# Performance work log

Measured on AMD Instinct MI355X. Metric: run time of the kernel, lower is better.

Reference implementation:

```python
import jax, jax.numpy as jnp
import numpy as np

B, L, C, H = 1, 2048, 2048, 16
D = C // H
EPS = 1e-6
W0 = 30.0  # SIREN frequency

def rmsnorm(x, w, eps=EPS):
    return x * jax.lax.rsqrt(jnp.mean(x * x, axis=-1, keepdims=True) + eps) * w

def depth_rope(x, depth, base=10000.0):
    # same rotation for all positions, angle set by scalar layer depth
    d = x.shape[-1]
    half = d // 2
    freqs = 1.0 / base ** (jnp.arange(half, dtype=x.dtype) / half)
    ang = depth * freqs
    cos, sin = jnp.cos(ang), jnp.sin(ang)
    x1, x2 = x[..., :half], x[..., half:2 * half]
    return jnp.concatenate([x1 * cos - x2 * sin, x1 * sin + x2 * cos], axis=-1)

def setup_inputs() -> dict:
    key = jax.random.key(0)
    ks = jax.random.split(key, 13)
    s = 1.0 / np.sqrt(C)
    inp = {
        'x':  jax.random.normal(ks[0], (B, L, C), jnp.float32),
        'h0': jax.random.normal(ks[1], (B, L, C), jnp.float32),
        'h1': jax.random.normal(ks[2], (B, L, C), jnp.float32),
        'h2': jax.random.normal(ks[3], (B, L, C), jnp.float32),
        'Wq': jax.random.normal(ks[4], (C, C), jnp.float32) * s,
        'Wk': jax.random.normal(ks[5], (C, C), jnp.float32) * s,
        'Wv': jax.random.normal(ks[6], (C, C), jnp.float32) * s,
        'Wo': jax.random.normal(ks[7], (C, C), jnp.float32) * s,
        'qn_w': jnp.ones((D,), jnp.float32),
        'kn_w': jnp.ones((D,), jnp.float32),
        'on_w': jnp.ones((C,), jnp.float32),
        'sw1': jax.random.normal(ks[8], (1, C), jnp.float32),
        'sb1': jax.random.normal(ks[9], (C,), jnp.float32) * 0.01,
        'sw2': jax.random.normal(ks[10], (C, C), jnp.float32) * s,
        'sb2': jnp.zeros((C,), jnp.float32),
    }
    return inp

def reference(x, h0, h1, h2, Wq, Wk, Wv, Wo, qn_w, kn_w, on_w, sw1, sb1, sw2, sb2):
    history = [h0, h1, h2]
    q_src = history[-1]                      # [B,L,C]
    q_depth = len(history) - 1
    # Q path: proj -> per-head RMSNorm -> depth RoPE
    q = jnp.einsum('blc,oc->blo', q_src, Wq).reshape(B, L, H, D)
    q = depth_rope(rmsnorm(q, qn_w), q_depth)
    # K/V path over prior history entries (each with its own depth)
    k_parts, v_parts = [], []
    for depth_idx, kv in enumerate(history[:-1]):
        k_i = jnp.einsum('blc,oc->blo', kv, Wk).reshape(B, L, H, D)
        v_i = jnp.einsum('blc,oc->blo', kv, Wv).reshape(B, L, H, D)
        k_parts.append(depth_rope(rmsnorm(k_i, kn_w), depth_idx))
        v_parts.append(v_i)
    k = jnp.concatenate(k_parts, axis=1)     # [B,Lkv,H,D]
    v = jnp.concatenate(v_parts, axis=1)
    # full SDPA, default scale D^-0.5
    scores = jnp.einsum('bqhd,bkhd->bhqk', q, k) * (D ** -0.5)
    attn = jax.nn.softmax(scores, axis=-1)
    out = jnp.einsum('bhqk,bkhd->bqhd', attn, v).reshape(B, L, C)
    out = jnp.einsum('blc,oc->blo', out, Wo)
    # SIREN upsample to (L,): target length == L -> identity interpolation
    # plus sine-activated coordinate MLP (implicit positional field)
    coords = jnp.linspace(-1.0, 1.0, L, dtype=x.dtype)[:, None]   # [L,1]
    pos = jnp.sin(W0 * (coords @ sw1 + sb1)) @ sw2 + sb2           # [L,C]
    out = out + pos[None]
    return x + rmsnorm(out, on_w)
```

## Files before the change

kernel.cpp:

```cpp
#include <hip/hip_runtime.h>
#include <hip/hip_fp16.h>

#define LQ 2048
#define CDIM 2048
#define NHEAD 16
#define HDIM 128
#define LKEY 4096

typedef _Float16 f16x8 __attribute__((ext_vector_type(8)));
typedef float f32x4 __attribute__((ext_vector_type(4)));

#define GLOAD_LDS16(g, s) __builtin_amdgcn_global_load_lds( \
    (const __attribute__((address_space(1))) void*)(g),     \
    (__attribute__((address_space(3))) void*)(s), 16, 0, 0)

#define MFMA16(a, b, c) __builtin_amdgcn_mfma_f32_16x16x32_f16(a, b, c, 0, 0, 0)

__device__ __forceinline__ void storeC(float* p, float v) { *p = v; }
__device__ __forceinline__ void storeC(__half* p, float v) { *p = __float2half(v); }
__device__ __forceinline__ float toF(float v) { return v; }
__device__ __forceinline__ float toF(__half v) { return __half2float(v); }

template <typename OutT>
__global__ __launch_bounds__(256, 2) void gemm_bt(
    const __half* __restrict__ A, const __half* __restrict__ B,
    OutT* __restrict__ C, int lda, int ldb, int ldc, int K)
{
    __shared__ __align__(16) __half lA[128 * 64];
    __shared__ __align__(16) __half lB[128 * 64];
    const int tid  = threadIdx.x;
    const int lane = tid & 63;
    const int wave = tid >> 6;
    const int bm = blockIdx.x, bn = blockIdx.y;
    const int r = tid >> 3;
    const int g = tid & 7;
    const __half* gA = A + (long)(bm * 128 + r) * lda + ((g ^ (r & 7)) << 3);
    const __half* gB = B + (long)(bn * 128 + r) * ldb + ((g ^ (r & 7)) << 3);
    __half* lAp = lA + tid * 8;
    __half* lBp = lB + tid * 8;
    const int wr = (wave & 1) << 6;
    const int wc = (wave >> 1) << 6;
    const int l15 = lane & 15, quad = lane >> 4;

    f32x4 acc[4][4] = {};

    for (int kt = 0; kt < K; kt += 64) {
#pragma unroll
        for (int i = 0; i < 4; ++i) {
            GLOAD_LDS16(gA + (long)i * 32 * lda, lAp + i * 2048);
            GLOAD_LDS16(gB + (long)i * 32 * ldb, lBp + i * 2048);
        }
        gA += 64; gB += 64;
        __syncthreads();
#pragma unroll
        for (int kk = 0; kk < 2; ++kk) {
            f16x8 af[4], bfr[4];
#pragma unroll
            for (int mi = 0; mi < 4; ++mi) {
                const int m = wr + mi * 16 + l15;
                const int kg = kk * 4 + quad;
                af[mi] = *(const f16x8*)&lA[m * 64 + ((kg ^ (m & 7)) << 3)];
            }
#pragma unroll
            for (int ni = 0; ni < 4; ++ni) {
                const int n = wc + ni * 16 + l15;
                const int kg = kk * 4 + quad;
                bfr[ni] = *(const f16x8*)&lB[n * 64 + ((kg ^ (n & 7)) << 3)];
            }
#pragma unroll
            for (int mi = 0; mi < 4; ++mi)
#pragma unroll
                for (int ni = 0; ni < 4; ++ni)
                    acc[mi][ni] = MFMA16(af[mi], bfr[ni], acc[mi][ni]);
        }
        __syncthreads();
    }
    const int row0 = bm * 128 + wr + quad * 4;
    const int col0 = bn * 128 + wc + l15;
#pragma unroll
    for (int mi = 0; mi < 4; ++mi)
#pragma unroll
        for (int ni = 0; ni < 4; ++ni)
#pragma unroll
            for (int rx = 0; rx < 4; ++rx)
                storeC(&C[(long)(row0 + mi * 16 + rx) * ldc + col0 + ni * 16],
                       acc[mi][ni][rx]);
}

__global__ __launch_bounds__(256, 2) void attn_tile(
    const __half* __restrict__ Qf,
    const __half* __restrict__ Kf,
    const __half* __restrict__ Vt,
    float* __restrict__ Opart,
    float* __restrict__ lsum)
{
    __shared__ __align__(16) __half lK[64 * 128];
    __shared__ __align__(16) __half lV[128 * 64];
    __shared__ __align__(16) __half pL[4 * 2 * 16 * 72];

    const int tid  = threadIdx.x;
    const int lane = tid & 63;
    const int wave = tid >> 6;
    const int l15  = lane & 15;
    const int quad = lane >> 4;
    const int h  = blockIdx.y >> 1;
    const int kc = blockIdx.y & 1;
    const int q0 = blockIdx.x * 128 + wave * 32;

    f16x8 aq[2][4];
#pragma unroll
    for (int mt = 0; mt < 2; ++mt)
#pragma unroll
        for (int ks = 0; ks < 4; ++ks)
            aq[mt][ks] = *(const f16x8*)&Qf[(long)(q0 + mt * 16 + l15) * CDIM +
                                            h * HDIM + ks * 32 + quad * 8];

    const int rK = tid >> 4;
    const int gK = tid & 15;
    const __half* srcK = Kf + (long)(kc * 2048 + rK) * 4096 + h * HDIM +
                         ((gK ^ (rK & 15)) << 3);
    const int rV = tid >> 3;
    const int gV = tid & 7;
    const __half* srcV = Vt + (long)(h * HDIM + rV) * (long)LKEY + kc * 2048 +
                         ((gV ^ (rV & 7)) << 3);
    __half* dstK = lK + tid * 8;
    __half* dstV = lV + tid * 8;

    f32x4 accO[2][8] = {};
    f32x4 l_acc[2] = {};

    for (int st = 0; st < 32; ++st) {
#pragma unroll
        for (int i = 0; i < 4; ++i) {
            GLOAD_LDS16(srcK + (long)(st * 64 + i * 16) * 4096, dstK + i * 2048);
            GLOAD_LDS16(srcV + (long)i * 32 * LKEY + st * 64, dstV + i * 2048);
        }
        __syncthreads();
        f32x4 s[2][4];
#pragma unroll
        for (int mt = 0; mt < 2; ++mt)
#pragma unroll
            for (int nt = 0; nt < 4; ++nt)
                s[mt][nt] = (f32x4){-10.f, -10.f, -10.f, -10.f};
#pragma unroll
        for (int nt = 0; nt < 4; ++nt) {
            const int n = nt * 16 + l15;
#pragma unroll
            for (int ks = 0; ks < 4; ++ks) {
                const f16x8 kf = *(const f16x8*)
                    &lK[n * 128 + (((ks * 4 + quad) ^ (n & 15)) << 3)];
                s[0][nt] = MFMA16(aq[0][ks], kf, s[0][nt]);
                s[1][nt] = MFMA16(aq[1][ks], kf, s[1][nt]);
            }
        }
#pragma unroll
        for (int mt = 0; mt < 2; ++mt)
#pragma unroll
            for (int nt = 0; nt < 4; ++nt)
#pragma unroll
                for (int r2 = 0; r2 < 4; ++r2) {
                    const float p = __builtin_amdgcn_exp2f(s[mt][nt][r2]);
                    l_acc[mt][r2] += p;
                    pL[((wave * 2 + mt) * 16 + quad * 4 + r2) * 72 +
                       nt * 16 + l15] = __float2half(p);
                }
        f16x8 ap[2][2];
#pragma unroll
        for (int mt = 0; mt < 2; ++mt) {
            ap[mt][0] = *(const f16x8*)&pL[((wave * 2 + mt) * 16 + l15) * 72 + quad * 8];
            ap[mt][1] = *(const f16x8*)&pL[((wave * 2 + mt) * 16 + l15) * 72 + 32 + quad * 8];
        }
#pragma unroll
        for (int nt2 = 0; nt2 < 8; ++nt2) {
            const int n2 = nt2 * 16 + l15;
            const f16x8 v0 = *(const f16x8*)&lV[n2 * 64 + ((quad ^ (n2 & 7)) << 3)];
            const f16x8 v1 = *(const f16x8*)&lV[n2 * 64 + (((4 + quad) ^ (n2 & 7)) << 3)];
            accO[0][nt2] = MFMA16(ap[0][0], v0, accO[0][nt2]);
            accO[0][nt2] = MFMA16(ap[0][1], v1, accO[0][nt2]);
            accO[1][nt2] = MFMA16(ap[1][0], v0, accO[1][nt2]);
            accO[1][nt2] = MFMA16(ap[1][1], v1, accO[1][nt2]);
        }
        __syncthreads();
    }

#pragma unroll
    for (int mt = 0; mt < 2; ++mt)
#pragma unroll
        for (int r2 = 0; r2 < 4; ++r2) {
            float v = l_acc[mt][r2];
            v += __shfl_xor(v, 1);
            v += __shfl_xor(v, 2);
            v += __shfl_xor(v, 4);
            v += __shfl_xor(v, 8);
            if (l15 == 0)
                atomicAdd(&lsum[h * LQ + q0 + mt * 16 + quad * 4 + r2], v);
        }
    float* Cp = Opart + (long)kc * LQ * CDIM + h * HDIM;
#pragma unroll
    for (int mt = 0; mt < 2; ++mt)
#pragma unroll
        for (int nt2 = 0; nt2 < 8; ++nt2)
#pragma unroll
            for (int rx = 0; rx < 4; ++rx)
                Cp[(long)(q0 + mt * 16 + quad * 4 + rx) * CDIM + nt2 * 16 + l15] =
                    accO[mt][nt2][rx];
}

__global__ __launch_bounds__(256) void merge_o(
    const float* __restrict__ Op, const float* __restrict__ lsum,
    __half* __restrict__ a2)
{
    const int row = blockIdx.x;
    const int c0  = threadIdx.x * 8;
    const float inv = 1.0f / lsum[(c0 >> 7) * LQ + row];
    const float* p0 = Op + (long)row * CDIM + c0;
    const float* p1 = p0 + (long)LQ * CDIM;
    union { f16x8 v; _Float16 e[8]; } o;
#pragma unroll
    for (int j = 0; j < 8; ++j)
        o.e[j] = (_Float16)((p0[j] + p1[j]) * inv);
    *(f16x8*)&a2[(long)row * 4096 + c0] = o.v;
}

__global__ __launch_bounds__(256) void norm_rope(
    __half* __restrict__ X, const float* __restrict__ w,
    int stride, int nrows, int kmode, float oscale)
{
    const int gid  = blockIdx.x * 4 + (threadIdx.x >> 6);
    const int lane = threadIdx.x & 63;
    const int row  = gid >> 4;
    const int h    = gid & 15;
    if (row >= nrows) return;
    __half* p = X + (long)row * stride + h * HDIM;
    float x1 = __half2float(p[lane]);
    float x2 = __half2float(p[lane + 64]);
    float ss = x1 * x1 + x2 * x2;
#pragma unroll
    for (int off = 1; off < 64; off <<= 1) ss += __shfl_xor(ss, off);
    const float rn = rsqrtf(ss * (1.0f / 128.0f) + 1e-6f);
    x1 *= rn * w[lane];
    x2 *= rn * w[lane + 64];
    const int depth = kmode ? (row < LQ ? 0 : 1) : 2;
    const float freq = exp2f(-(float)lane * 0.20762050593045702f);
    const float ang = (float)depth * freq;
    float sn, cs;
    __sincosf(ang, &sn, &cs);
    p[lane]      = __float2half((x1 * cs - x2 * sn) * oscale);
    p[lane + 64] = __float2half((x1 * sn + x2 * cs) * oscale);
}

__global__ void cast_h4(const float* __restrict__ in, __half* __restrict__ out, int n) {
    const int i = (blockIdx.x * 256 + threadIdx.x) << 2;
    if (i >= n) return;
    const float4 v = *(const float4*)&in[i];
    out[i]     = __float2half(v.x);
    out[i + 1] = __float2half(v.y);
    out[i + 2] = __float2half(v.z);
    out[i + 3] = __float2half(v.w);
}

__global__ void cast_wo(const float* __restrict__ in, __half* __restrict__ out) {
    const int idx = blockIdx.x * 256 + threadIdx.x;
    const int o = idx >> 11, c = idx & 2047;
    out[((long)o << 12) + c] = __float2half(in[idx]);
}

template <typename InT>
__global__ __launch_bounds__(256) void transpose_h(
    const InT* __restrict__ in, long inStride, long inOff,
    __half* __restrict__ out, long outStride, long outOff)
{
    __shared__ float t[64][65];
    const long r0 = (long)blockIdx.x * 64;
    const long c0 = (long)blockIdx.y * 64;
    const int tj = threadIdx.x & 63;
    const int ti = threadIdx.x >> 6;
#pragma unroll
    for (int it = 0; it < 16; ++it) {
        const int i = it * 4 + ti;
        t[i][tj] = toF(in[(r0 + i) * inStride + inOff + c0 + tj]);
    }
    __syncthreads();
#pragma unroll
    for (int it = 0; it < 16; ++it) {
        const int i = it * 4 + ti;
        out[(c0 + i) * outStride + outOff + r0 + tj] = __float2half(t[tj][i]);
    }
}

__global__ void sin_feat(const float* __restrict__ sw1, const float* __restrict__ sb1,
                         __half* __restrict__ a2) {
    const int idx = blockIdx.x * 256 + threadIdx.x;
    const int l = idx >> 11, c = idx & 2047;
    const float coord = -1.0f + (2.0f / 2047.0f) * (float)l;
    const float v = sinf(30.0f * (coord * sw1[c] + sb1[c]));
    a2[((long)l << 12) + 2048 + c] = __float2half(v);
}

__global__ __launch_bounds__(256) void final_norm(
    const float* __restrict__ out2, const float* __restrict__ x,
    const float* __restrict__ sb2, const float* __restrict__ on_w,
    float* __restrict__ y)
{
    const int row = blockIdx.x;
    const float* o = out2 + (long)row * CDIM;
    float v[8];
    float ss = 0.f;
#pragma unroll
    for (int i = 0; i < 8; ++i) {
        const int c = threadIdx.x + i * 256;
        const float t = o[c] + sb2[c];
        v[i] = t;
        ss += t * t;
    }
#pragma unroll
    for (int off = 1; off < 64; off <<= 1) ss += __shfl_xor(ss, off);
    __shared__ float red[4];
    const int lane = threadIdx.x & 63, wv = threadIdx.x >> 6;
    if (lane == 0) red[wv] = ss;
    __syncthreads();
    const float tot = red[0] + red[1] + red[2] + red[3];
    const float rn = rsqrtf(tot * (1.0f / 2048.0f) + 1e-6f);
#pragma unroll
    for (int i = 0; i < 8; ++i) {
        const int c = threadIdx.x + i * 256;
        y[(long)row * CDIM + c] = x[(long)row * CDIM + c] + v[i] * rn * on_w[c];
    }
}

extern "C" void kernel_launch(void* const* d_in, const int* in_sizes, int n_in,
                              void* d_out, int out_size, void* d_ws, size_t ws_size,
                              hipStream_t stream) {
    const float* x    = (const float*)d_in[0];
    const float* h0   = (const float*)d_in[1];
    const float* h1   = (const float*)d_in[2];
    const float* h2   = (const float*)d_in[3];
    const float* Wq   = (const float*)d_in[4];
    const float* Wk   = (const float*)d_in[5];
    const float* Wv   = (const float*)d_in[6];
    const float* Wo   = (const float*)d_in[7];
    const float* qn_w = (const float*)d_in[8];
    const float* kn_w = (const float*)d_in[9];
    const float* on_w = (const float*)d_in[10];
    const float* sw1  = (const float*)d_in[11];
    const float* sb1  = (const float*)d_in[12];
    const float* sw2  = (const float*)d_in[13];
    const float* sb2  = (const float*)d_in[14];
    float* y = (float*)d_out;

    const size_t MB = 1ull << 20;
    char* w = (char*)d_ws;
    __half* xq  = (__half*)(w);
    __half* xkv = (__half*)(w + 8 * MB);
    __half* wqh = (__half*)(w + 24 * MB);
    __half* wkv = (__half*)(w + 32 * MB);
    __half* qf  = (__half*)(w + 48 * MB);
    __half* kvf = (__half*)(w + 56 * MB);
    __half* vT  = (__half*)(w + 88 * MB);
    __half* a2  = (__half*)(w + 104 * MB);
    __half* b2  = (__half*)(w + 120 * MB);
    float* out2 = (float*)(w + 136 * MB);
    float* Opart = (float*)(w);
    float* lsum  = (float*)(w + 32 * MB);
    (void)in_sizes; (void)n_in; (void)out_size; (void)ws_size;

    const int n4 = 2048 * 2048;
    cast_h4<<<n4 / 1024, 256, 0, stream>>>(h2, xq, n4);
    cast_h4<<<n4 / 1024, 256, 0, stream>>>(h0, xkv, n4);
    cast_h4<<<n4 / 1024, 256, 0, stream>>>(h1, xkv + n4, n4);
    cast_h4<<<n4 / 1024, 256, 0, stream>>>(Wq, wqh, n4);
    cast_h4<<<n4 / 1024, 256, 0, stream>>>(Wk, wkv, n4);
    cast_h4<<<n4 / 1024, 256, 0, stream>>>(Wv, wkv + n4, n4);
    cast_wo<<<n4 / 256, 256, 0, stream>>>(Wo, b2);
    transpose_h<float><<<dim3(32, 32), 256, 0, stream>>>(sw2, 2048, 0, b2, 4096, 2048);
    sin_feat<<<n4 / 256, 256, 0, stream>>>(sw1, sb1, a2);

    gemm_bt<__half><<<dim3(16, 16), 256, 0, stream>>>(xq, wqh, qf, 2048, 2048, 2048, 2048);
    gemm_bt<__half><<<dim3(32, 32), 256, 0, stream>>>(xkv, wkv, kvf, 2048, 2048, 4096, 2048);

    norm_rope<<<8192, 256, 0, stream>>>(qf, qn_w, 2048, 2048, 0, 0.12751743f);
    norm_rope<<<16384, 256, 0, stream>>>(kvf, kn_w, 4096, 4096, 1, 1.0f);
    transpose_h<__half><<<dim3(64, 32), 256, 0, stream>>>(kvf, 4096, 2048, vT, 4096, 0);

    (void)hipMemsetAsync(lsum, 0, NHEAD * LQ * sizeof(float), stream);
    attn_tile<<<dim3(16, 32), 256, 0, stream>>>(qf, kvf, vT, Opart, lsum);
    merge_o<<<2048, 256, 0, stream>>>(Opart, lsum, a2);

    gemm_bt<float><<<dim3(16, 16), 256, 0, stream>>>(a2, b2, out2, 4096, 4096, 2048, 4096);
    final_norm<<<2048, 256, 0, stream>>>(out2, x, sb2, on_w, y);
}
```

Baseline: 525.9 us.

## Halve attention query tile, reuse K LDS for P, raise occupancy and swizzle blocks

The attention kernel now gives each wave 16 query rows instead of 32, doubling the grid to 1024 blocks, and raises launch bounds to four blocks per CU. The separate P staging buffer is dropped and the K tile's LDS is reused for P after an extra barrier, which cuts LDS per block. Block indices are remapped so neighbouring blocks cover different head/key-chunk pairs on the same query tile. The aim is more waves in flight to hide the exp/LDS latency, at the cost of loading each K/V tile twice as often from global memory and an extra sync per iteration.

```diff
diff --git a/kernel.cpp b/kernel.cpp
--- a/kernel.cpp
+++ b/kernel.cpp
@@ -87,7 +87,7 @@
                        acc[mi][ni][rx]);
 }
 
-__global__ __launch_bounds__(256, 2) void attn_tile(
+__global__ __launch_bounds__(256, 4) void attn_tile(
     const __half* __restrict__ Qf,
     const __half* __restrict__ Kf,
     const __half* __restrict__ Vt,
@@ -96,24 +96,24 @@
 {
     __shared__ __align__(16) __half lK[64 * 128];
     __shared__ __align__(16) __half lV[128 * 64];
-    __shared__ __align__(16) __half pL[4 * 2 * 16 * 72];
 
     const int tid  = threadIdx.x;
     const int lane = tid & 63;
     const int wave = tid >> 6;
     const int l15  = lane & 15;
     const int quad = lane >> 4;
-    const int h  = blockIdx.y >> 1;
-    const int kc = blockIdx.y & 1;
-    const int q0 = blockIdx.x * 128 + wave * 32;
-
-    f16x8 aq[2][4];
-#pragma unroll
-    for (int mt = 0; mt < 2; ++mt)
-#pragma unroll
-        for (int ks = 0; ks < 4; ++ks)
-            aq[mt][ks] = *(const f16x8*)&Qf[(long)(q0 + mt * 16 + l15) * CDIM +
-                                            h * HDIM + ks * 32 + quad * 8];
+    const int lin = blockIdx.y * 32 + blockIdx.x;
+    const int hkc = (lin & 7) * 4 + ((lin >> 3) & 3);
+    const int qt  = lin >> 5;
+    const int h   = hkc >> 1;
+    const int kc  = hkc & 1;
+    const int q0  = qt * 64 + wave * 16;
+
+    f16x8 aq[4];
+#pragma unroll
+    for (int ks = 0; ks < 4; ++ks)
+        aq[ks] = *(const f16x8*)&Qf[(long)(q0 + l15) * CDIM +
+                                    h * HDIM + ks * 32 + quad * 8];
 
     const int rK = tid >> 4;
     const int gK = tid & 15;
@@ -125,9 +125,10 @@
                          ((gV ^ (rV & 7)) << 3);
     __half* dstK = lK + tid * 8;
     __half* dstV = lV + tid * 8;
-
-    f32x4 accO[2][8] = {};
-    f32x4 l_acc[2] = {};
+    __half* pW = lK + wave * (16 * 76);
+
+    f32x4 accO[8] = {};
+    f32x4 l_acc = {};
 
     for (int st = 0; st < 32; ++st) {
 #pragma unroll
@@ -136,12 +137,10 @@
             GLOAD_LDS16(srcV + (long)i * 32 * LKEY + st * 64, dstV + i * 2048);
         }
         __syncthreads();
-        f32x4 s[2][4];
-#pragma unroll
-        for (int mt = 0; mt < 2; ++mt)
-#pragma unroll
-            for (int nt = 0; nt < 4; ++nt)
-                s[mt][nt] = (f32x4){-10.f, -10.f, -10.f, -10.f};
+        f32x4 s[4];
+#pragma unroll
+        for (int nt = 0; nt < 4; ++nt)
+            s[nt] = (f32x4){-10.f, -10.f, -10.f, -10.f};
 #pragma unroll
         for (int nt = 0; nt < 4; ++nt) {
             const int n = nt * 16 + l15;
@@ -149,61 +148,48 @@
             for (int ks = 0; ks < 4; ++ks) {
                 const f16x8 kf = *(const f16x8*)
                     &lK[n * 128 + (((ks * 4 + quad) ^ (n & 15)) << 3)];
-                s[0][nt] = MFMA16(aq[0][ks], kf, s[0][nt]);
-                s[1][nt] = MFMA16(aq[1][ks], kf, s[1][nt]);
+                s[nt] = MFMA16(aq[ks], kf, s[nt]);
             }
         }
-#pragma unroll
-        for (int mt = 0; mt < 2; ++mt)
-#pragma unroll
-            for (int nt = 0; nt < 4; ++nt)
-#pragma unroll
-                for (int r2 = 0; r2 < 4; ++r2) {
-                    const float p = __builtin_amdgcn_exp2f(s[mt][nt][r2]);
-                    l_acc[mt][r2] += p;
-                    pL[((wave * 2 + mt) * 16 + quad * 4 + r2) * 72 +
-                       nt * 16 + l15] = __float2half(p);
-                }
-        f16x8 ap[2][2];
-#pragma unroll
-        for (int mt = 0; mt < 2; ++mt) {
-            ap[mt][0] = *(const f16x8*)&pL[((wave * 2 + mt) * 16 + l15) * 72 + quad * 8];
-            ap[mt][1] = *(const f16x8*)&pL[((wave * 2 + mt) * 16 + l15) * 72 + 32 + quad * 8];
-        }
+        __syncthreads();
+#pragma unroll
+        for (int nt = 0; nt < 4; ++nt)
+#pragma unroll
+            for (int r2 = 0; r2 < 4; ++r2) {
+                const float p = __builtin_amdgcn_exp2f(s[nt][r2]);
+                l_acc[r2] += p;
+                pW[(quad * 4 + r2) * 76 + nt * 16 + l15] = __float2half(p);
+            }
+        f16x8 ap0 = *(const f16x8*)&pW[l15 * 76 + quad * 8];
+        f16x8 ap1 = *(const f16x8*)&pW[l15 * 76 + 32 + quad * 8];
 #pragma unroll
         for (int nt2 = 0; nt2 < 8; ++nt2) {
             const int n2 = nt2 * 16 + l15;
             const f16x8 v0 = *(const f16x8*)&lV[n2 * 64 + ((quad ^ (n2 & 7)) << 3)];
             const f16x8 v1 = *(const f16x8*)&lV[n2 * 64 + (((4 + quad) ^ (n2 & 7)) << 3)];
-            accO[0][nt2] = MFMA16(ap[0][0], v0, accO[0][nt2]);
-            accO[0][nt2] = MFMA16(ap[0][1], v1, accO[0][nt2]);
-            accO[1][nt2] = MFMA16(ap[1][0], v0, accO[1][nt2]);
-            accO[1][nt2] = MFMA16(ap[1][1], v1, accO[1][nt2]);
-        }
-        __syncthreads();
-    }
-
-#pragma unroll
-    for (int mt = 0; mt < 2; ++mt)
-#pragma unroll
-        for (int r2 = 0; r2 < 4; ++r2) {
-            float v = l_acc[mt][r2];
-            v += __shfl_xor(v, 1);
-            v += __shfl_xor(v, 2);
-            v += __shfl_xor(v, 4);
-            v += __shfl_xor(v, 8);
-            if (l15 == 0)
-                atomicAdd(&lsum[h * LQ + q0 + mt * 16 + quad * 4 + r2], v);
-        }
+            accO[nt2] = MFMA16(ap0, v0, accO[nt2]);
+            accO[nt2] = MFMA16(ap1, v1, accO[nt2]);
+        }
+        __syncthreads();
+    }
+
+#pragma unroll
+    for (int r2 = 0; r2 < 4; ++r2) {
+        float v = l_acc[r2];
+        v += __shfl_xor(v, 1);
+        v += __shfl_xor(v, 2);
+        v += __shfl_xor(v, 4);
+        v += __shfl_xor(v, 8);
+        if (l15 == 0)
+            atomicAdd(&lsum[h * LQ + q0 + quad * 4 + r2], v);
+    }
     float* Cp = Opart + (long)kc * LQ * CDIM + h * HDIM;
 #pragma unroll
-    for (int mt = 0; mt < 2; ++mt)
-#pragma unroll
-        for (int nt2 = 0; nt2 < 8; ++nt2)
-#pragma unroll
-            for (int rx = 0; rx < 4; ++rx)
-                Cp[(long)(q0 + mt * 16 + quad * 4 + rx) * CDIM + nt2 * 16 + l15] =
-                    accO[mt][nt2][rx];
+    for (int nt2 = 0; nt2 < 8; ++nt2)
+#pragma unroll
+        for (int rx = 0; rx < 4; ++rx)
+            Cp[(long)(q0 + quad * 4 + rx) * CDIM + nt2 * 16 + l15] =
+                accO[nt2][rx];
 }
 
 __global__ __launch_bounds__(256) void merge_o(
@@ -383,7 +369,7 @@
     transpose_h<__half><<<dim3(64, 32), 256, 0, stream>>>(kvf, 4096, 2048, vT, 4096, 0);
 
     (void)hipMemsetAsync(lsum, 0, NHEAD * LQ * sizeof(float), stream);
-    attn_tile<<<dim3(16, 32), 256, 0, stream>>>(qf, kvf, vT, Opart, lsum);
+    attn_tile<<<dim3(32, 32), 256, 0, stream>>>(qf, kvf, vT, Opart, lsum);
     merge_o<<<2048, 256, 0, stream>>>(Opart, lsum, a2);
 
     gemm_bt<float><<<dim3(16, 16), 256, 0, stream>>>(a2, b2, out2, 4096, 4096, 2048, 4096);
```

Result: no change. 533.7 us (+1.5%).

## Enlarge attention query tile to 64 rows per wave and remap block order

Applied to the files above, without the earlier changes.

Each wave in the attention kernel now processes 64 query rows instead of 32, so each K/V tile loaded into LDS feeds twice as much MFMA work. The grid is halved, and blocks are linearly remapped so neighbouring blocks work on different head/key-chunk pairs. V fragments are preloaded into registers once per step and reused across the four query subtiles, and the P staging buffer is reused per subtile. The cost is higher register pressure (launch bounds dropped to 1 block per CU) and fewer blocks (256) on a large GPU, which reduces occupancy and latency hiding.

```diff
diff --git a/kernel.cpp b/kernel.cpp
--- a/kernel.cpp
+++ b/kernel.cpp
@@ -87,7 +87,7 @@
                        acc[mi][ni][rx]);
 }
 
-__global__ __launch_bounds__(256, 2) void attn_tile(
+__global__ __launch_bounds__(256, 1) void attn_tile(
     const __half* __restrict__ Qf,
     const __half* __restrict__ Kf,
     const __half* __restrict__ Vt,
@@ -96,20 +96,23 @@
 {
     __shared__ __align__(16) __half lK[64 * 128];
     __shared__ __align__(16) __half lV[128 * 64];
-    __shared__ __align__(16) __half pL[4 * 2 * 16 * 72];
+    __shared__ __align__(16) __half pL[4 * 16 * 76];
 
     const int tid  = threadIdx.x;
     const int lane = tid & 63;
     const int wave = tid >> 6;
     const int l15  = lane & 15;
     const int quad = lane >> 4;
-    const int h  = blockIdx.y >> 1;
-    const int kc = blockIdx.y & 1;
-    const int q0 = blockIdx.x * 128 + wave * 32;
-
-    f16x8 aq[2][4];
-#pragma unroll
-    for (int mt = 0; mt < 2; ++mt)
+    const int lin = blockIdx.y * 8 + blockIdx.x;
+    const int hkc = (lin & 7) * 4 + ((lin >> 3) & 3);
+    const int qt  = lin >> 5;
+    const int h   = hkc >> 1;
+    const int kc  = hkc & 1;
+    const int q0  = qt * 256 + wave * 64;
+
+    f16x8 aq[4][4];
+#pragma unroll
+    for (int mt = 0; mt < 4; ++mt)
 #pragma unroll
         for (int ks = 0; ks < 4; ++ks)
             aq[mt][ks] = *(const f16x8*)&Qf[(long)(q0 + mt * 16 + l15) * CDIM +
@@ -125,9 +128,10 @@
                          ((gV ^ (rV & 7)) << 3);
     __half* dstK = lK + tid * 8;
     __half* dstV = lV + tid * 8;
-
-    f32x4 accO[2][8] = {};
-    f32x4 l_acc[2] = {};
+    __half* pW = pL + wave * (16 * 76);
+
+    f32x4 accO[4][8] = {};
+    f32x4 l_acc[4] = {};
 
     for (int st = 0; st < 32; ++st) {
 #pragma unroll
@@ -136,9 +140,9 @@
             GLOAD_LDS16(srcV + (long)i * 32 * LKEY + st * 64, dstV + i * 2048);
         }
         __syncthreads();
-        f32x4 s[2][4];
-#pragma unroll
-        for (int mt = 0; mt < 2; ++mt)
+        f32x4 s[4][4];
+#pragma unroll
+        for (int mt = 0; mt < 4; ++mt)
 #pragma unroll
             for (int nt = 0; nt < 4; ++nt)
                 s[mt][nt] = (f32x4){-10.f, -10.f, -10.f, -10.f};
@@ -149,42 +153,41 @@
             for (int ks = 0; ks < 4; ++ks) {
                 const f16x8 kf = *(const f16x8*)
                     &lK[n * 128 + (((ks * 4 + quad) ^ (n & 15)) << 3)];
-                s[0][nt] = MFMA16(aq[0][ks], kf, s[0][nt]);
-                s[1][nt] = MFMA16(aq[1][ks], kf, s[1][nt]);
+#pragma unroll
+                for (int mt = 0; mt < 4; ++mt)
+                    s[mt][nt] = MFMA16(aq[mt][ks], kf, s[mt][nt]);
             }
         }
-#pragma unroll
-        for (int mt = 0; mt < 2; ++mt)
+        f16x8 vr[16];
+#pragma unroll
+        for (int nt2 = 0; nt2 < 8; ++nt2) {
+            const int n2 = nt2 * 16 + l15;
+            vr[2 * nt2]     = *(const f16x8*)&lV[n2 * 64 + ((quad ^ (n2 & 7)) << 3)];
+            vr[2 * nt2 + 1] = *(const f16x8*)&lV[n2 * 64 + (((4 + quad) ^ (n2 & 7)) << 3)];
+        }
+#pragma unroll
+        for (int mt = 0; mt < 4; ++mt) {
 #pragma unroll
             for (int nt = 0; nt < 4; ++nt)
 #pragma unroll
                 for (int r2 = 0; r2 < 4; ++r2) {
                     const float p = __builtin_amdgcn_exp2f(s[mt][nt][r2]);
                     l_acc[mt][r2] += p;
-                    pL[((wave * 2 + mt) * 16 + quad * 4 + r2) * 72 +
-                       nt * 16 + l15] = __float2half(p);
+                    pW[(quad * 4 + r2) * 76 + nt * 16 + l15] = __float2half(p);
                 }
-        f16x8 ap[2][2];
-#pragma unroll
-        for (int mt = 0; mt < 2; ++mt) {
-            ap[mt][0] = *(const f16x8*)&pL[((wave * 2 + mt) * 16 + l15) * 72 + quad * 8];
-            ap[mt][1] = *(const f16x8*)&pL[((wave * 2 + mt) * 16 + l15) * 72 + 32 + quad * 8];
-        }
-#pragma unroll
-        for (int nt2 = 0; nt2 < 8; ++nt2) {
-            const int n2 = nt2 * 16 + l15;
-            const f16x8 v0 = *(const f16x8*)&lV[n2 * 64 + ((quad ^ (n2 & 7)) << 3)];
-            const f16x8 v1 = *(const f16x8*)&lV[n2 * 64 + (((4 + quad) ^ (n2 & 7)) << 3)];
-            accO[0][nt2] = MFMA16(ap[0][0], v0, accO[0][nt2]);
-            accO[0][nt2] = MFMA16(ap[0][1], v1, accO[0][nt2]);
-            accO[1][nt2] = MFMA16(ap[1][0], v0, accO[1][nt2]);
-            accO[1][nt2] = MFMA16(ap[1][1], v1, accO[1][nt2]);
+            const f16x8 ap0 = *(const f16x8*)&pW[l15 * 76 + quad * 8];
+            const f16x8 ap1 = *(const f16x8*)&pW[l15 * 76 + 32 + quad * 8];
+#pragma unroll
+            for (int nt2 = 0; nt2 < 8; ++nt2) {
+                accO[mt][nt2] = MFMA16(ap0, vr[2 * nt2],     accO[mt][nt2]);
+                accO[mt][nt2] = MFMA16(ap1, vr[2 * nt2 + 1], accO[mt][nt2]);
+            }
         }
         __syncthreads();
     }
 
 #pragma unroll
-    for (int mt = 0; mt < 2; ++mt)
+    for (int mt = 0; mt < 4; ++mt)
 #pragma unroll
         for (int r2 = 0; r2 < 4; ++r2) {
             float v = l_acc[mt][r2];
@@ -197,7 +200,7 @@
         }
     float* Cp = Opart + (long)kc * LQ * CDIM + h * HDIM;
 #pragma unroll
-    for (int mt = 0; mt < 2; ++mt)
+    for (int mt = 0; mt < 4; ++mt)
 #pragma unroll
         for (int nt2 = 0; nt2 < 8; ++nt2)
 #pragma unroll
@@ -383,7 +386,7 @@
     transpose_h<__half><<<dim3(64, 32), 256, 0, stream>>>(kvf, 4096, 2048, vT, 4096, 0);
 
     (void)hipMemsetAsync(lsum, 0, NHEAD * LQ * sizeof(float), stream);
-    attn_tile<<<dim3(16, 32), 256, 0, stream>>>(qf, kvf, vT, Opart, lsum);
+    attn_tile<<<dim3(8, 32), 256, 0, stream>>>(qf, kvf, vT, Opart, lsum);
     merge_o<<<2048, 256, 0, stream>>>(Opart, lsum, a2);
 
     gemm_bt<float><<<dim3(16, 16), 256, 0, stream>>>(a2, b2, out2, 4096, 4096, 2048, 4096);
```

Result: slower. 562.7 us (+7.0%).
